# Performance work log

Hardware: AMD Instinct MI355X
Metric: run time of the kernel (lower is better)

## Reference

```python
import jax, jax.numpy as jnp
import numpy as np

N = 100000   # nodes
E = 640000   # edges
G = 256      # graphs in batch
L = 3        # mpnn layers
D_IN = 64    # in_node_channels
E_IN = 16    # in_edge_channels
H = 128      # hidden width (uniform)


def setup_inputs() -> dict:
    key = jax.random.key(0)
    ks = jax.random.split(key, 20)
    s = 0.05
    inp = {
        "x": jax.random.normal(ks[0], (N, D_IN), dtype=jnp.float32),
        "edge_index": jax.random.randint(ks[1], (2, E), 0, N, dtype=jnp.int64),
        "edge_attr": jax.random.normal(ks[2], (E, E_IN), dtype=jnp.float32),
        "batch_vec": jnp.sort(jax.random.randint(ks[3], (N,), 0, G, dtype=jnp.int64)),
        # input encoders
        "Wn0": jax.random.normal(ks[4], (D_IN, H), dtype=jnp.float32) * s,
        "bn0": jnp.zeros((H,), jnp.float32),
        "We0": jax.random.normal(ks[5], (E_IN, H), dtype=jnp.float32) * s,
        "be0": jnp.zeros((H,), jnp.float32),
        # per-layer MPNN params (stacked over L)
        "WM": jax.random.normal(ks[6], (L, 3 * H, H), dtype=jnp.float32) * s,
        "bM": jnp.zeros((L, H), jnp.float32),
        "WU": jax.random.normal(ks[7], (L, 2 * H, H), dtype=jnp.float32) * s,
        "bU": jnp.zeros((L, H), jnp.float32),
        # per-layer node/edge linear layers
        "Wn": jax.random.normal(ks[8], (L, H, H), dtype=jnp.float32) * s,
        "bn": jnp.zeros((L, H), jnp.float32),
        "We": jax.random.normal(ks[9], (L, H, H), dtype=jnp.float32) * s,
        "be": jnp.zeros((L, H), jnp.float32),
        "Wh": jax.random.normal(ks[10], (H, 1), dtype=jnp.float32) * s,
        "bh": jnp.zeros((1,), jnp.float32),
    }
    return inp


def _mpnn_layer(x, edge_attr, src, dst, WM, bM, WU, bU):
    # message: relu(Linear([x_i, x_j, e]))  (x_i = target, x_j = source)
    xi = x[dst]                                   # [E, H]
    xj = x[src]                                   # [E, H]
    m = jax.nn.relu(jnp.concatenate([xi, xj, edge_attr], axis=-1) @ WM + bM)
    # mean aggregation at target nodes
    agg = jax.ops.segment_sum(m, dst, num_segments=N)        # [N, H]
    cnt = jax.ops.segment_sum(jnp.ones((m.shape[0], 1), x.dtype), dst,
                              num_segments=N)
    agg = agg / jnp.maximum(cnt, 1.0)
    # update: relu(Linear([x, aggr_out]))
    return jax.nn.relu(jnp.concatenate([x, agg], axis=-1) @ WU + bU)


def reference(x, edge_index, edge_attr, batch_vec,
              Wn0, bn0, We0, be0, WM, bM, WU, bU, Wn, bn, We, be, Wh, bh):
    src, dst = edge_index[0], edge_index[1]       # PyG source_to_target flow
    h = jax.nn.relu(x @ Wn0 + bn0)                # NodeFeatureLinear
    e = jax.nn.relu(edge_attr @ We0 + be0)        # EdgeFeatureLinear
    for i in range(L):
        h = _mpnn_layer(h, e, src, dst, WM[i], bM[i], WU[i], bU[i])
        h = jax.nn.relu(h @ Wn[i] + bn[i])
        e = jax.nn.relu(e @ We[i] + be[i])
    # global mean pool over graphs
    sums = jax.ops.segment_sum(h, batch_vec, num_segments=G)  # [G, H]
    cnts = jax.ops.segment_sum(jnp.ones((N, 1), h.dtype), batch_vec,
                               num_segments=G)
    pooled = sums / jnp.maximum(cnts, 1.0)
    return pooled @ Wh + bh                       # [G, 1]
```

## Files before the change

### kernel.cpp

```cpp
#include <hip/hip_runtime.h>

#define NN 100000
#define EE 640000
#define GG 256
#define LL 3
#define HH 128

constexpr int BM = 64;
constexpr int BK = 16;

typedef _Float16 f16;
typedef f16 f16x8 __attribute__((ext_vector_type(8)));
typedef f16 f16x4 __attribute__((ext_vector_type(4)));
typedef f16 f16x2 __attribute__((ext_vector_type(2)));
typedef float f32x4 __attribute__((ext_vector_type(4)));

#define TSTR 136

__device__ __forceinline__ void gload_lds16(const void* g, void* l) {
  __builtin_amdgcn_global_load_lds(
      (const __attribute__((address_space(1))) void*)g,
      (__attribute__((address_space(3))) void*)l, 16, 0, 0);
}

template <int MODE>
__global__ __launch_bounds__(256) void gemm_k(
    const float* __restrict__ X, const float* __restrict__ W,
    const float* __restrict__ bias, float* __restrict__ out, int M, int K,
    const float* __restrict__ X2, const float* __restrict__ inv) {
  __shared__ __align__(16) float Xs[BK][BM];
  __shared__ __align__(16) float Ws[BK][HH];

  const int tid = threadIdx.x;
  const int m0 = blockIdx.x * BM;
  const int tm = (tid >> 4) << 2;
  const int tn = (tid & 15) << 3;
  const int xr = tid >> 2;
  const int xc = (tid & 3) << 2;

  float acc[4][8];
#pragma unroll
  for (int i = 0; i < 4; ++i)
#pragma unroll
    for (int j = 0; j < 8; ++j) acc[i][j] = 0.f;

  for (int k0 = 0; k0 < K; k0 += BK) {
    float4 xv = make_float4(0.f, 0.f, 0.f, 0.f);
    if (m0 + xr < M) {
      if (MODE == 3) {
        if (k0 < HH) {
          xv = *(const float4*)(X + (size_t)(m0 + xr) * HH + k0 + xc);
        } else {
          xv = *(const float4*)(X2 + (size_t)(m0 + xr) * HH + (k0 - HH) + xc);
          const float s = inv[m0 + xr];
          xv.x *= s; xv.y *= s; xv.z *= s; xv.w *= s;
        }
      } else {
        xv = *(const float4*)(X + (size_t)(m0 + xr) * K + k0 + xc);
      }
    }
    Xs[xc + 0][xr] = xv.x;
    Xs[xc + 1][xr] = xv.y;
    Xs[xc + 2][xr] = xv.z;
    Xs[xc + 3][xr] = xv.w;
#pragma unroll
    for (int i = 0; i < 2; ++i) {
      const int q = tid + i * 256;
      const int row = q >> 5;
      const int c4 = (q & 31) << 2;
      *(float4*)&Ws[row][c4] =
          *(const float4*)(W + (size_t)(k0 + row) * HH + c4);
    }
    __syncthreads();
#pragma unroll
    for (int k = 0; k < BK; ++k) {
      const float4 x4 = *(const float4*)&Xs[k][tm];
      const float4 w0 = *(const float4*)&Ws[k][tn];
      const float4 w1 = *(const float4*)&Ws[k][tn + 4];
      const float xr_[4] = {x4.x, x4.y, x4.z, x4.w};
      const float wr_[8] = {w0.x, w0.y, w0.z, w0.w, w1.x, w1.y, w1.z, w1.w};
#pragma unroll
      for (int i = 0; i < 4; ++i)
#pragma unroll
        for (int j = 0; j < 8; ++j)
          acc[i][j] = fmaf(xr_[i], wr_[j], acc[i][j]);
    }
    __syncthreads();
  }

#pragma unroll
  for (int i = 0; i < 4; ++i) {
    const int r = m0 + tm + i;
    if (r >= M) continue;
    float o[8];
#pragma unroll
    for (int j = 0; j < 8; ++j) {
      float v = acc[i][j];
      if (MODE == 1 || MODE == 3) {
        v += bias[tn + j];
        v = v > 0.f ? v : 0.f;
      }
      o[j] = v;
    }
    float4* d4 = (float4*)(out + (size_t)r * HH + tn);
    d4[0] = make_float4(o[0], o[1], o[2], o[3]);
    d4[1] = make_float4(o[4], o[5], o[6], o[7]);
  }
}

__global__ void prep_w(const float* __restrict__ We0,
                       const float* __restrict__ We,
                       const float* __restrict__ WM,
                       const float* __restrict__ Wn0,
                       const float* __restrict__ Wn,
                       const float* __restrict__ WU, f16* __restrict__ out) {
  const int buf = blockIdx.x >> 3;
  const int rowg = blockIdx.x & 7;
  const float* src;
  int K;
  if (buf == 0) {
    src = We0; K = 16;
  } else if (buf <= 2) {
    src = We + (size_t)(buf - 1) * HH * HH; K = HH;
  } else if (buf <= 5) {
    src = WM + (size_t)(buf - 3) * 3 * HH * HH + 2 * HH * HH; K = HH;
  } else if (buf == 6) {
    src = Wn0; K = 64;
  } else if (buf <= 9) {
    src = WM + (size_t)(buf - 7) * 3 * HH * HH; K = HH;
  } else if (buf <= 12) {
    src = WM + (size_t)(buf - 10) * 3 * HH * HH + HH * HH; K = HH;
  } else if (buf <= 15) {
    src = Wn + (size_t)(buf - 13) * HH * HH; K = HH;
  } else {
    const int t = buf - 16;
    src = WU + (size_t)(t >> 1) * 2 * HH * HH + (size_t)(t & 1) * HH * HH;
    K = HH;
  }
  f16* dst = out + (size_t)buf * HH * TSTR;
  for (int idx = threadIdx.x; idx < 16 * TSTR; idx += 256) {
    const int n = rowg * 16 + idx / TSTR;
    const int k = idx % TSTR;
    const float v = (k < K) ? src[(size_t)k * HH + n] : 0.f;
    dst[(size_t)n * TSTR + k] = (f16)v;
  }
}

template <int MODE>
__global__ __launch_bounds__(256) void gemm_mfma(
    const float* __restrict__ X, const f16* __restrict__ WT,
    const float* __restrict__ bias, float* __restrict__ out, int M,
    const float* __restrict__ X2, const float* __restrict__ inv,
    const f16* __restrict__ WT2, float* __restrict__ out2) {
  __shared__ __align__(16) char smem[17408 + 34816];
  f16* Xs = (f16*)smem;
  f16* Wt = (f16*)(smem + 17408);
  float* V = (float*)(smem + 17408);

  const int tid = threadIdx.x;
  const int lane = tid & 63;
  const int wv = tid >> 6;
  const int l15 = lane & 15;
  const int q = lane >> 4;
  const int m0 = blockIdx.x * 64;

  f32x4 acc[4][2];
#pragma unroll
  for (int mi = 0; mi < 4; ++mi)
#pragma unroll
    for (int ni = 0; ni < 2; ++ni) {
      f32x4 z = {};
      acc[mi][ni] = z;
    }

  auto stageX = [&](const float* Xp, int stride, int KC, bool scale) {
    const int npr = KC >> 2;
    for (int i = tid; i < 64 * npr; i += 256) {
      const int row = i / npr;
      const int c4 = (i - row * npr) << 2;
      float4 v = make_float4(0.f, 0.f, 0.f, 0.f);
      if (m0 + row < M) {
        v = *(const float4*)(Xp + (size_t)(m0 + row) * stride + c4);
        if (scale) {
          const float s = inv[m0 + row];
          v.x *= s; v.y *= s; v.z *= s; v.w *= s;
        }
      }
      f16x4 hv;
      hv[0] = (f16)v.x; hv[1] = (f16)v.y; hv[2] = (f16)v.z; hv[3] = (f16)v.w;
      *(f16x4*)&Xs[(size_t)row * TSTR + c4] = hv;
    }
  };

  auto stageW = [&](const f16* Wg) {
    const char* g = (const char*)Wg;
    char* l = (char*)Wt;
#pragma unroll
    for (int i = 0; i < 8; ++i)
      gload_lds16(g + tid * 16 + i * 4096, l + tid * 16 + i * 4096);
    if (tid < 128) gload_lds16(g + tid * 16 + 32768, l + tid * 16 + 32768);
  };

  auto mfmaN = [&](f32x4 (&ac)[4][2], int nk) {
    for (int kk = 0; kk < nk; ++kk) {
      f16x8 a[4], b[2];
#pragma unroll
      for (int mi = 0; mi < 4; ++mi)
        a[mi] = *(const f16x8*)&Xs[(size_t)(mi * 16 + l15) * TSTR + kk * 32 +
                                   q * 8];
#pragma unroll
      for (int ni = 0; ni < 2; ++ni)
        b[ni] = *(const f16x8*)&Wt[(size_t)((wv * 2 + ni) * 16 + l15) * TSTR +
                                   kk * 32 + q * 8];
#pragma unroll
      for (int mi = 0; mi < 4; ++mi)
#pragma unroll
        for (int ni = 0; ni < 2; ++ni)
          ac[mi][ni] = __builtin_amdgcn_mfma_f32_16x16x32_f16(
              a[mi], b[ni], ac[mi][ni], 0, 0, 0);
    }
  };

  auto dumpV = [&](f32x4 (&ac)[4][2], const float* bp) {
    float bv0 = 0.f, bv1 = 0.f;
    if (bp) { bv0 = bp[wv * 32 + l15]; bv1 = bp[wv * 32 + 16 + l15]; }
#pragma unroll
    for (int mi = 0; mi < 4; ++mi)
#pragma unroll
      for (int ni = 0; ni < 2; ++ni)
#pragma unroll
        for (int rr = 0; rr < 4; ++rr) {
          float v = ac[mi][ni][rr];
          if (bp) {
            v += ni ? bv1 : bv0;
            v = v > 0.f ? v : 0.f;
          }
          V[(size_t)(mi * 16 + q * 4 + rr) * 132 + wv * 32 + ni * 16 + l15] =
              v;
        }
  };

  auto storeV = [&](float* op) {
    const int tm = (tid >> 4) << 2;
    const int tn = (tid & 15) << 3;
#pragma unroll
    for (int i = 0; i < 4; ++i) {
      const int r = m0 + tm + i;
      if (r >= M) continue;
      float4* d = (float4*)(op + (size_t)r * HH + tn);
      d[0] = *(const float4*)&V[(size_t)(tm + i) * 132 + tn];
      d[1] = *(const float4*)&V[(size_t)(tm + i) * 132 + tn + 4];
    }
  };

  auto storeV16 = [&](f16* op) {
    const int tm = (tid >> 4) << 2;
    const int tn = (tid & 15) << 3;
#pragma unroll
    for (int i = 0; i < 4; ++i) {
      const int r = m0 + tm + i;
      if (r >= M) continue;
      const float* vp = &V[(size_t)(tm + i) * 132 + tn];
      f16x8 hv;
#pragma unroll
      for (int j = 0; j < 8; ++j) hv[j] = (f16)vp[j];
      *(f16x8*)(op + (size_t)r * HH + tn) = hv;
    }
  };

  if constexpr (MODE == 2) {
    stageW(WT);
    stageX(X, 64, 64, false);
    __syncthreads();
    mfmaN(acc, 2);
    __syncthreads();
    dumpV(acc, bias);
    __syncthreads();
    storeV(out);
  } else if constexpr (MODE == 1) {
    stageW(WT);
    stageX(X, HH, 128, false);
    __syncthreads();
    mfmaN(acc, 4);
    __syncthreads();
    dumpV(acc, bias);
    __syncthreads();
    storeV(out);
  } else if constexpr (MODE == 3) {
    stageW(WT);
    stageX(X, HH, 128, false);
    __syncthreads();
    mfmaN(acc, 4);
    __syncthreads();
    stageW(WT + (size_t)HH * TSTR);
    stageX(X2, HH, 128, true);
    __syncthreads();
    mfmaN(acc, 4);
    __syncthreads();
    dumpV(acc, bias);
    __syncthreads();
    storeV(out);
  } else {
    f32x4 acc2[4][2];
#pragma unroll
    for (int mi = 0; mi < 4; ++mi)
#pragma unroll
      for (int ni = 0; ni < 2; ++ni) {
        f32x4 z = {};
        acc2[mi][ni] = z;
      }
    stageW(WT);
    stageX(X, HH, 128, false);
    __syncthreads();
    mfmaN(acc, 4);
    __syncthreads();
    stageW(WT2);
    __syncthreads();
    mfmaN(acc2, 4);
    __syncthreads();
    dumpV(acc, nullptr);
    __syncthreads();
    storeV16((f16*)out);
    __syncthreads();
    dumpV(acc2, nullptr);
    __syncthreads();
    storeV16((f16*)out2);
  }
}

template <int CHAIN>
__global__ __launch_bounds__(256) void msg_k(
    const float* __restrict__ ea, const f16* __restrict__ W0T,
    const float* __restrict__ be0, const f16* __restrict__ WeT,
    const float* __restrict__ beL, const f16* __restrict__ WMeT,
    const float* __restrict__ bMl, const f16* __restrict__ A,
    const f16* __restrict__ B, const int* __restrict__ sIdx,
    const int* __restrict__ sSrc, const int* __restrict__ sDst,
    float* __restrict__ agg) {
  __shared__ __align__(16) char smem[17408 + 34816 + 256];
  f16* Tc = (f16*)smem;
  f16* Wc = (f16*)(smem + 17408);
  float* V = (float*)(smem + 17408);
  int* dstS = (int*)(smem + 17408 + 34816);

  const int tid = threadIdx.x;
  const int lane = tid & 63;
  const int wv = tid >> 6;
  const int l15 = lane & 15;
  const int q = lane >> 4;
  const int r0 = blockIdx.x * 64;

  auto wptr = [&](int p) -> const f16* {
    if (p == 0) return W0T;
    if (p <= CHAIN) return WeT + (size_t)(p - 1) * HH * TSTR;
    return WMeT;
  };

  auto stage_w = [&](const f16* Wg) {
    const char* g = (const char*)Wg;
    char* l = (char*)Wc;
#pragma unroll
    for (int i = 0; i < 8; ++i)
      gload_lds16(g + tid * 16 + i * 4096, l + tid * 16 + i * 4096);
    if (tid < 128) gload_lds16(g + tid * 16 + 32768, l + tid * 16 + 32768);
  };

  stage_w(wptr(0));
  {
    const int xr = tid >> 2;
    const int xc = (tid & 3) << 2;
    const int e = sIdx[r0 + xr];
    const float4 v = *(const float4*)(ea + (size_t)e * 16 + xc);
    f16x4 hv;
    hv[0] = (f16)v.x; hv[1] = (f16)v.y; hv[2] = (f16)v.z; hv[3] = (f16)v.w;
    *(f16x4*)&Tc[(size_t)xr * TSTR + xc] = hv;
    f16x4 z = {};
    *(f16x4*)&Tc[(size_t)xr * TSTR + 16 + xc] = z;
    if (tid < 64) dstS[tid] = sDst[r0 + tid];
  }

  f32x4 acc[4][2];

  auto zero_acc = [&]() {
#pragma unroll
    for (int mi = 0; mi < 4; ++mi)
#pragma unroll
      for (int ni = 0; ni < 2; ++ni) {
        f32x4 z = {};
        acc[mi][ni] = z;
      }
  };

  auto mfma_steps = [&](int nk) {
    for (int kk = 0; kk < nk; ++kk) {
      f16x8 a[4], b[2];
#pragma unroll
      for (int mi = 0; mi < 4; ++mi)
        a[mi] = *(const f16x8*)&Tc[(size_t)(mi * 16 + l15) * TSTR + kk * 32 +
                                   q * 8];
#pragma unroll
      for (int ni = 0; ni < 2; ++ni)
        b[ni] = *(const f16x8*)&Wc[(size_t)((wv * 2 + ni) * 16 + l15) * TSTR +
                                   kk * 32 + q * 8];
#pragma unroll
      for (int mi = 0; mi < 4; ++mi)
#pragma unroll
        for (int ni = 0; ni < 2; ++ni)
          acc[mi][ni] = __builtin_amdgcn_mfma_f32_16x16x32_f16(
              a[mi], b[ni], acc[mi][ni], 0, 0, 0);
    }
  };

  auto relu_body = [&](const float* bias) {
    float bv0 = bias[wv * 32 + l15];
    float bv1 = bias[wv * 32 + 16 + l15];
#pragma unroll
    for (int mi = 0; mi < 4; ++mi)
#pragma unroll
      for (int ni = 0; ni < 2; ++ni) {
        const float bb = ni ? bv1 : bv0;
#pragma unroll
        for (int rr = 0; rr < 4; ++rr) {
          float v = acc[mi][ni][rr] + bb;
          v = v > 0.f ? v : 0.f;
          Tc[(size_t)(mi * 16 + q * 4 + rr) * TSTR + wv * 32 + ni * 16 + l15] =
              (f16)v;
        }
      }
  };

  zero_acc();
  __syncthreads();
  mfma_steps(1);
  __syncthreads();
  stage_w(wptr(1));
  relu_body(be0);
  __syncthreads();

#pragma unroll
  for (int s = 0; s < CHAIN; ++s) {
    zero_acc();
    mfma_steps(4);
    __syncthreads();
    stage_w(wptr(s + 2));
    relu_body(beL + (size_t)s * HH);
    __syncthreads();
  }

  zero_acc();
  mfma_steps(4);
  __syncthreads();

#pragma unroll
  for (int mi = 0; mi < 4; ++mi)
#pragma unroll
    for (int ni = 0; ni < 2; ++ni)
#pragma unroll
      for (int rr = 0; rr < 4; ++rr)
        V[(size_t)(mi * 16 + q * 4 + rr) * 129 + wv * 32 + ni * 16 + l15] =
            acc[mi][ni][rr];
  __syncthreads();

  const int tm = (tid >> 4) << 2;
  const int tn = (tid & 15) << 3;
  const float4 m0v = *(const float4*)(bMl + tn);
  const float4 m1v = *(const float4*)(bMl + tn + 4);
  const float mv[8] = {m0v.x, m0v.y, m0v.z, m0v.w,
                       m1v.x, m1v.y, m1v.z, m1v.w};
#pragma unroll
  for (int i = 0; i < 4; ++i) {
    const int rr = r0 + tm + i;
    const int d = dstS[tm + i];
    const int s = sSrc[rr];
    const f16x8 a8 = *(const f16x8*)(A + (size_t)d * HH + tn);
    const f16x8 b8 = *(const f16x8*)(B + (size_t)s * HH + tn);
    float* vp = &V[(size_t)(tm + i) * 129 + tn];
#pragma unroll
    for (int j = 0; j < 8; ++j)
      vp[j] = fmaxf(vp[j] + (float)a8[j] + (float)b8[j] + mv[j], 0.f);
  }
  __syncthreads();

  const int c = tid & 127;
  const int h = tid >> 7;
  float racc = 0.f;
  int cur = dstS[h * 32];
  bool first = true;
  for (int e2 = h * 32; e2 < h * 32 + 32; ++e2) {
    const int d = dstS[e2];
    if (d != cur) {
      if (first) {
        atomicAdd(&agg[(size_t)cur * HH + c], racc);
        first = false;
      } else {
        agg[(size_t)cur * HH + c] = racc;
      }
      racc = 0.f;
      cur = d;
    }
    racc += V[(size_t)e2 * 129 + c];
  }
  atomicAdd(&agg[(size_t)cur * HH + c], racc);
}

__global__ void count_kernel(const int* __restrict__ dst, int* cnt, int E) {
  const int i = blockIdx.x * 256 + threadIdx.x;
  if (i < E) atomicAdd(&cnt[dst[i]], 1);
}

__global__ void invcnt_kernel(const int* __restrict__ cnt, float* inv, int n) {
  const int i = blockIdx.x * 256 + threadIdx.x;
  if (i < n) inv[i] = 1.0f / (float)max(cnt[i], 1);
}

__global__ void scan_block(const int* __restrict__ cnt, int* excl, int* bsum,
                           int n) {
  __shared__ int s[256];
  const int tx = threadIdx.x;
  const int i = blockIdx.x * 256 + tx;
  const int v = (i < n) ? cnt[i] : 0;
  s[tx] = v;
  __syncthreads();
  for (int off = 1; off < 256; off <<= 1) {
    int tv = (tx >= off) ? s[tx - off] : 0;
    __syncthreads();
    s[tx] += tv;
    __syncthreads();
  }
  if (i < n) excl[i] = s[tx] - v;
  if (tx == 255) bsum[blockIdx.x] = s[255];
}

__global__ __launch_bounds__(512) void scan_bsum(int* bsum, int nb) {
  __shared__ int s[512];
  const int t = threadIdx.x;
  const int v0 = (t < nb) ? bsum[t] : 0;
  s[t] = v0;
  __syncthreads();
  for (int off = 1; off < 512; off <<= 1) {
    const int tv = (t >= off) ? s[t - off] : 0;
    __syncthreads();
    s[t] += tv;
    __syncthreads();
  }
  if (t < nb) bsum[t] = s[t] - v0;
}

__global__ void scan_add(int* excl, const int* __restrict__ bsum, int n) {
  const int i = blockIdx.x * 256 + threadIdx.x;
  if (i < n) excl[i] += bsum[blockIdx.x];
}

__global__ void scatter_edges(const int* __restrict__ dst,
                              const int* __restrict__ src,
                              const int* __restrict__ off, int* ctr, int* sIdx,
                              int* sSrc, int* sDst, int E) {
  const int e = blockIdx.x * 256 + threadIdx.x;
  if (e >= E) return;
  const int d = dst[e];
  const int p = off[d] + atomicAdd(&ctr[d], 1);
  sIdx[p] = e;
  sSrc[p] = src[e];
  sDst[p] = d;
}

__global__ void pool_accum(const float* __restrict__ h,
                           const int* __restrict__ batch,
                           float* __restrict__ gsum, int M) {
  const int col = threadIdx.x;
  const int r0 = blockIdx.x * 64;
  const int rend = min(r0 + 64, M);
  if (r0 >= M) return;
  float acc = 0.f;
  int cur = batch[r0];
  for (int r = r0; r < rend; ++r) {
    const int b = batch[r];
    if (b != cur) {
      atomicAdd(&gsum[(size_t)cur * HH + col], acc);
      acc = 0.f;
      cur = b;
    }
    acc += h[(size_t)r * HH + col];
  }
  atomicAdd(&gsum[(size_t)cur * HH + col], acc);
}

__global__ void gcnt_kernel(const int* __restrict__ batch, int* gcnt, int n) {
  const int i = blockIdx.x * 256 + threadIdx.x;
  if (i < n) atomicAdd(&gcnt[batch[i]], 1);
}

__global__ void head_kernel(const float* __restrict__ gsum,
                            const int* __restrict__ gcnt,
                            const float* __restrict__ Wh,
                            const float* __restrict__ bh,
                            float* __restrict__ out) {
  const int g = blockIdx.x;
  const int t = threadIdx.x;
  float v = gsum[(size_t)g * HH + t] * Wh[t];
#pragma unroll
  for (int o = 32; o > 0; o >>= 1) v += __shfl_down(v, o, 64);
  __shared__ float red[2];
  if ((t & 63) == 0) red[t >> 6] = v;
  __syncthreads();
  if (t == 0) {
    const float s = red[0] + red[1];
    const float c = (float)max(gcnt[g], 1);
    out[g] = s / c + bh[0];
  }
}

extern "C" void kernel_launch(void* const* d_in, const int* in_sizes, int n_in,
                              void* d_out, int out_size, void* d_ws,
                              size_t ws_size, hipStream_t stream) {
  (void)in_sizes; (void)n_in; (void)out_size;
  const float* x = (const float*)d_in[0];
  const int* ei = (const int*)d_in[1];
  const float* ea = (const float*)d_in[2];
  const int* batch = (const int*)d_in[3];
  const float* Wn0 = (const float*)d_in[4];
  const float* bn0 = (const float*)d_in[5];
  const float* We0 = (const float*)d_in[6];
  const float* be0 = (const float*)d_in[7];
  const float* WM = (const float*)d_in[8];
  const float* bM = (const float*)d_in[9];
  const float* WU = (const float*)d_in[10];
  const float* bU = (const float*)d_in[11];
  const float* Wn = (const float*)d_in[12];
  const float* bn = (const float*)d_in[13];
  const float* We = (const float*)d_in[14];
  const float* be = (const float*)d_in[15];
  const float* Wh = (const float*)d_in[16];
  const float* bh = (const float*)d_in[17];

  const int* srcI = ei;
  const int* dstI = ei + EE;

  float* w = (float*)d_ws;
  size_t o = 0;
  float* h = w + o;    o += (size_t)NN * HH;
  float* agg = w + o;  o += (size_t)NN * HH;
  f16* A16 = (f16*)(w + o); o += (size_t)NN * HH / 2;
  f16* B16 = (f16*)(w + o); o += (size_t)NN * HH / 2;
  float* gsum = w + o; o += (size_t)GG * HH;
  float* invc = w + o; o += (size_t)NN;
  int* cnt = (int*)(w + o);  o += (size_t)NN;
  int* gcnt = (int*)(w + o); o += (size_t)GG;
  int* off = (int*)(w + o);  o += (size_t)NN;
  int* ctr = (int*)(w + o);  o += (size_t)NN;
  int* bsum = (int*)(w + o); o += 512;
  int* sIdx = (int*)(w + o); o += (size_t)EE;
  int* sSrc = (int*)(w + o); o += (size_t)EE;
  int* sDst = (int*)(w + o); o += (size_t)EE;
  f16* Wp = (f16*)(w + o);   o += (size_t)22 * HH * TSTR / 2;
  if (o * sizeof(float) > ws_size) return;

  auto WB = [&](int i) { return Wp + (size_t)i * HH * TSTR; };

  const dim3 blk(256);
  const int gridN = (NN + BM - 1) / BM;
  const int gridE = EE / BM;
  const int NBLK = (NN + 255) / 256;

  hipMemsetAsync(cnt, 0, (size_t)NN * sizeof(int), stream);
  hipMemsetAsync(ctr, 0, (size_t)NN * sizeof(int), stream);
  hipMemsetAsync(gsum, 0, (size_t)GG * HH * sizeof(float), stream);
  hipMemsetAsync(gcnt, 0, (size_t)GG * sizeof(int), stream);

  count_kernel<<<(EE + 255) / 256, blk, 0, stream>>>(dstI, cnt, EE);
  scan_block<<<NBLK, blk, 0, stream>>>(cnt, off, bsum, NN);
  scan_bsum<<<1, dim3(512), 0, stream>>>(bsum, NBLK);
  scan_add<<<NBLK, blk, 0, stream>>>(off, bsum, NN);
  scatter_edges<<<(EE + 255) / 256, blk, 0, stream>>>(dstI, srcI, off, ctr,
                                                      sIdx, sSrc, sDst, EE);
  invcnt_kernel<<<(NN + 255) / 256, blk, 0, stream>>>(cnt, invc, NN);
  prep_w<<<22 * 8, blk, 0, stream>>>(We0, We, WM, Wn0, Wn, WU, Wp);

  gemm_mfma<2><<<gridN, blk, 0, stream>>>(x, WB(6), bn0, h, NN, nullptr,
                                          nullptr, nullptr, nullptr);

  for (int l = 0; l < LL; ++l) {
    gemm_mfma<4><<<gridN, blk, 0, stream>>>(h, WB(7 + l), nullptr,
                                            (float*)A16, NN, nullptr, nullptr,
                                            WB(10 + l), (float*)B16);
    hipMemsetAsync(agg, 0, (size_t)NN * HH * sizeof(float), stream);
    switch (l) {
      case 0:
        msg_k<0><<<gridE, blk, 0, stream>>>(ea, WB(0), be0, WB(1), be, WB(3),
                                            bM + 0 * HH, A16, B16, sIdx, sSrc,
                                            sDst, agg);
        break;
      case 1:
        msg_k<1><<<gridE, blk, 0, stream>>>(ea, WB(0), be0, WB(1), be, WB(4),
                                            bM + 1 * HH, A16, B16, sIdx, sSrc,
                                            sDst, agg);
        break;
      default:
        msg_k<2><<<gridE, blk, 0, stream>>>(ea, WB(0), be0, WB(1), be, WB(5),
                                            bM + 2 * HH, A16, B16, sIdx, sSrc,
                                            sDst, agg);
        break;
    }
    gemm_mfma<3><<<gridN, blk, 0, stream>>>(h, WB(16 + 2 * l), bU + l * HH, h,
                                            NN, agg, invc, nullptr, nullptr);
    gemm_mfma<1><<<gridN, blk, 0, stream>>>(h, WB(13 + l), bn + l * HH, h, NN,
                                            nullptr, nullptr, nullptr,
                                            nullptr);
  }

  pool_accum<<<gridN, dim3(128), 0, stream>>>(h, batch, gsum, NN);
  gcnt_kernel<<<(NN + 255) / 256, blk, 0, stream>>>(batch, gcnt, NN);
  head_kernel<<<GG, dim3(128), 0, stream>>>(gsum, gcnt, Wh, bh, (float*)d_out);
}
```

Baseline: 1.163 ms.

## Double message kernel edge tile to 128 rows with 512-thread blocks

The per-edge message kernel now processes 128 sorted edges per block with 8 waves instead of 64 edges with 4 waves. Two groups of four waves share each staged weight matrix in LDS, so weights are loaded once per 128 edges rather than once per 64, halving weight staging traffic per edge. LDS use rises to about 70 KB per block, which may limit blocks per CU, and the unseen epilogue/scatter section must correctly handle 512 threads and 128 rows.

```diff
diff --git a/kernel.cpp b/kernel.cpp
--- a/kernel.cpp
+++ b/kernel.cpp
@@ -329,7 +329,7 @@
 }
 
 template <int CHAIN>
-__global__ __launch_bounds__(256) void msg_k(
+__global__ __launch_bounds__(512) void msg_k(
     const float* __restrict__ ea, const f16* __restrict__ W0T,
     const float* __restrict__ be0, const f16* __restrict__ WeT,
     const float* __restrict__ beL, const f16* __restrict__ WMeT,
@@ -337,18 +337,20 @@
     const f16* __restrict__ B, const int* __restrict__ sIdx,
     const int* __restrict__ sSrc, const int* __restrict__ sDst,
     float* __restrict__ agg) {
-  __shared__ __align__(16) char smem[17408 + 34816 + 256];
+  __shared__ __align__(16) char smem[34816 + 34816 + 512];
   f16* Tc = (f16*)smem;
-  f16* Wc = (f16*)(smem + 17408);
-  float* V = (float*)(smem + 17408);
-  int* dstS = (int*)(smem + 17408 + 34816);
+  f16* Wc = (f16*)(smem + 34816);
+  float* V = (float*)smem;
+  int* dstS = (int*)(smem + 69632);
 
   const int tid = threadIdx.x;
   const int lane = tid & 63;
   const int wv = tid >> 6;
+  const int ew = (wv >> 2) * 64;
+  const int wn = wv & 3;
   const int l15 = lane & 15;
   const int q = lane >> 4;
-  const int r0 = blockIdx.x * 64;
+  const int r0 = blockIdx.x * 128;
 
   auto wptr = [&](int p) -> const f16* {
     if (p == 0) return W0T;
@@ -360,8 +362,8 @@
     const char* g = (const char*)Wg;
     char* l = (char*)Wc;
 #pragma unroll
-    for (int i = 0; i < 8; ++i)
-      gload_lds16(g + tid * 16 + i * 4096, l + tid * 16 + i * 4096);
+    for (int i = 0; i < 4; ++i)
+      gload_lds16(g + tid * 16 + i * 8192, l + tid * 16 + i * 8192);
     if (tid < 128) gload_lds16(g + tid * 16 + 32768, l + tid * 16 + 32768);
   };
 
@@ -376,7 +378,7 @@
     *(f16x4*)&Tc[(size_t)xr * TSTR + xc] = hv;
     f16x4 z = {};
     *(f16x4*)&Tc[(size_t)xr * TSTR + 16 + xc] = z;
-    if (tid < 64) dstS[tid] = sDst[r0 + tid];
+    if (tid < 128) dstS[tid] = sDst[r0 + tid];
   }
 
   f32x4 acc[4][2];
@@ -396,11 +398,11 @@
       f16x8 a[4], b[2];
 #pragma unroll
       for (int mi = 0; mi < 4; ++mi)
-        a[mi] = *(const f16x8*)&Tc[(size_t)(mi * 16 + l15) * TSTR + kk * 32 +
-                                   q * 8];
+        a[mi] = *(const f16x8*)&Tc[(size_t)(ew + mi * 16 + l15) * TSTR +
+                                   kk * 32 + q * 8];
 #pragma unroll
       for (int ni = 0; ni < 2; ++ni)
-        b[ni] = *(const f16x8*)&Wc[(size_t)((wv * 2 + ni) * 16 + l15) * TSTR +
+        b[ni] = *(const f16x8*)&Wc[(size_t)((wn * 2 + ni) * 16 + l15) * TSTR +
                                    kk * 32 + q * 8];
 #pragma unroll
       for (int mi = 0; mi < 4; ++mi)
@@ -412,8 +414,8 @@
   };
 
   auto relu_body = [&](const float* bias) {
-    float bv0 = bias[wv * 32 + l15];
-    float bv1 = bias[wv * 32 + 16 + l15];
+    float bv0 = bias[wn * 32 + l15];
+    float bv1 = bias[wn * 32 + 16 + l15];
 #pragma unroll
     for (int mi = 0; mi < 4; ++mi)
 #pragma unroll
@@ -423,8 +425,8 @@
         for (int rr = 0; rr < 4; ++rr) {
           float v = acc[mi][ni][rr] + bb;
           v = v > 0.f ? v : 0.f;
-          Tc[(size_t)(mi * 16 + q * 4 + rr) * TSTR + wv * 32 + ni * 16 + l15] =
-              (f16)v;
+          Tc[(size_t)(ew + mi * 16 + q * 4 + rr) * TSTR + wn * 32 + ni * 16 +
+             l15] = (f16)v;
         }
       }
   };
@@ -457,8 +459,8 @@
     for (int ni = 0; ni < 2; ++ni)
 #pragma unroll
       for (int rr = 0; rr < 4; ++rr)
-        V[(size_t)(mi * 16 + q * 4 + rr) * 129 + wv * 32 + ni * 16 + l15] =
-            acc[mi][ni][rr];
+        V[(size_t)(ew + mi * 16 + q * 4 + rr) * 129 + wn * 32 + ni * 16 +
+          l15] = acc[mi][ni][rr];
   __syncthreads();
 
   const int tm = (tid >> 4) << 2;
@@ -659,7 +661,7 @@
 
   const dim3 blk(256);
   const int gridN = (NN + BM - 1) / BM;
-  const int gridE = EE / BM;
+  const int gridE = EE / 128;
   const int NBLK = (NN + 255) / 256;
 
   hipMemsetAsync(cnt, 0, (size_t)NN * sizeof(int), stream);
@@ -686,19 +688,19 @@
     hipMemsetAsync(agg, 0, (size_t)NN * HH * sizeof(float), stream);
     switch (l) {
       case 0:
-        msg_k<0><<<gridE, blk, 0, stream>>>(ea, WB(0), be0, WB(1), be, WB(3),
-                                            bM + 0 * HH, A16, B16, sIdx, sSrc,
-                                            sDst, agg);
+        msg_k<0><<<gridE, dim3(512), 0, stream>>>(
+            ea, WB(0), be0, WB(1), be, WB(3), bM + 0 * HH, A16, B16, sIdx,
+            sSrc, sDst, agg);
         break;
       case 1:
-        msg_k<1><<<gridE, blk, 0, stream>>>(ea, WB(0), be0, WB(1), be, WB(4),
-                                            bM + 1 * HH, A16, B16, sIdx, sSrc,
-                                            sDst, agg);
+        msg_k<1><<<gridE, dim3(512), 0, stream>>>(
+            ea, WB(0), be0, WB(1), be, WB(4), bM + 1 * HH, A16, B16, sIdx,
+            sSrc, sDst, agg);
         break;
       default:
-        msg_k<2><<<gridE, blk, 0, stream>>>(ea, WB(0), be0, WB(1), be, WB(5),
-                                            bM + 2 * HH, A16, B16, sIdx, sSrc,
-                                            sDst, agg);
+        msg_k<2><<<gridE, dim3(512), 0, stream>>>(
+            ea, WB(0), be0, WB(1), be, WB(5), bM + 2 * HH, A16, B16, sIdx,
+            sSrc, sDst, agg);
         break;
     }
     gemm_mfma<3><<<gridN, blk, 0, stream>>>(h, WB(16 + 2 * l), bU + l * HH, h,
```

After: 1.121 ms. -3.6%, faster.
